# Kernel tuning notes

Measured on AMD Instinct MI355X. Metric: run time of the kernel, lower is better.

The kernel has to match this reference:

```python
import math
import jax, jax.numpy as jnp
import numpy as np

B = 2
N = 48           # max_atoms
A = 16           # num_atom_types
E = 5            # num_bond_types
HID = 384
NH = 8
HD = HID // NH   # 48
LYR = 4
MLP = 4 * HID
L = N + N * N    # 2352 sequence length (nodes + flattened edges)


def setup_inputs() -> dict:
    key = jax.random.key(0)
    ks = iter(jax.random.split(key, 48))
    r = lambda *s: jax.random.normal(next(ks), s, jnp.float32) * 0.02
    d = {
        "x": jax.random.normal(next(ks), (B, N, A), jnp.float32),
        "adj": jax.random.normal(next(ks), (B, N, N, E), jnp.float32),
        "t": jax.random.uniform(next(ks), (B,), jnp.float32),
        # embeddings
        "node_w": r(A, HID), "node_b": jnp.zeros((HID,), jnp.float32),
        "edge_w": r(E, HID), "edge_b": jnp.zeros((HID,), jnp.float32),
        "pos": r(L, HID),
        # timestep MLP (SinusoidalPositionalEmbedding(HID) -> Linear(HID,4H) -> SiLU -> Linear(4H,H))
        "t_w1": r(HID, 4 * HID), "t_b1": jnp.zeros((4 * HID,), jnp.float32),
        "t_w2": r(4 * HID, HID), "t_b2": jnp.zeros((HID,), jnp.float32),
        # stacked per-layer params
        "ada1_w": r(LYR, HID, 2 * HID), "ada1_b": jnp.zeros((LYR, 2 * HID), jnp.float32),
        "ada2_w": r(LYR, HID, 2 * HID), "ada2_b": jnp.zeros((LYR, 2 * HID), jnp.float32),
        "q_w": r(LYR, HID, HID), "q_b": jnp.zeros((LYR, HID), jnp.float32),
        "k_w": r(LYR, HID, HID), "k_b": jnp.zeros((LYR, HID), jnp.float32),
        "v_w": r(LYR, HID, HID), "v_b": jnp.zeros((LYR, HID), jnp.float32),
        "o_w": r(LYR, HID, HID), "o_b": jnp.zeros((LYR, HID), jnp.float32),
        "m1_w": r(LYR, HID, MLP), "m1_b": jnp.zeros((LYR, MLP), jnp.float32),
        "m2_w": r(LYR, MLP, HID), "m2_b": jnp.zeros((LYR, HID), jnp.float32),
        # final norm + heads (heads random instead of zero-init so output is informative)
        "fn_g": jnp.ones((HID,), jnp.float32), "fn_b": jnp.zeros((HID,), jnp.float32),
        "on_w": r(HID, A), "on_b": jnp.zeros((A,), jnp.float32),
        "oe_w": r(HID, E), "oe_b": jnp.zeros((E,), jnp.float32),
    }
    return d


def _ln(z):
    # LayerNorm(elementwise_affine=False), eps=1e-5
    mu = z.mean(-1, keepdims=True)
    var = z.var(-1, keepdims=True)
    return (z - mu) * jax.lax.rsqrt(var + 1e-5)


def _forward(x, adj, t, node_w, node_b, edge_w, edge_b, pos,
             t_w1, t_b1, t_w2, t_b2,
             ada1_w, ada1_b, ada2_w, ada2_b,
             q_w, q_b, k_w, k_b, v_w, v_b, o_w, o_b,
             m1_w, m1_b, m2_w, m2_b,
             fn_g, fn_b, on_w, on_b, oe_w, oe_b):
    b = x.shape[0]
    # embed nodes and edges, concat into sequence [b, L, HID]
    h_nodes = x @ node_w + node_b                       # [b, N, H]
    h_edges = adj.reshape(b, N * N, E) @ edge_w + edge_b  # [b, N*N, H]
    h = jnp.concatenate([h_nodes, h_edges], axis=1) + pos[None]
    # sinusoidal timestep embedding -> cond [b, HID]
    half = HID // 2
    freqs = jnp.exp(-math.log(10000.0) * jnp.arange(half, dtype=jnp.float32) / half)
    ang = t[:, None].astype(jnp.float32) * freqs[None, :]
    temb = jnp.concatenate([jnp.sin(ang), jnp.cos(ang)], axis=-1)
    cond = jax.nn.silu(temb @ t_w1 + t_b1) @ t_w2 + t_b2
    inv_scale = 1.0 / math.sqrt(HD)
    for i in range(LYR):
        # AdaLN 1 + attention
        sc, sh = jnp.split(cond @ ada1_w[i] + ada1_b[i], 2, axis=-1)
        n = _ln(h) * (1.0 + sc[:, None, :]) + sh[:, None, :]
        q = (n @ q_w[i] + q_b[i]).reshape(b, L, NH, HD)
        k = (n @ k_w[i] + k_b[i]).reshape(b, L, NH, HD)
        v = (n @ v_w[i] + v_b[i]).reshape(b, L, NH, HD)
        scores = jnp.einsum('bqhd,bkhd->bhqk', q, k) * inv_scale
        attn = jax.nn.softmax(scores, axis=-1)
        ao = jnp.einsum('bhqk,bkhd->bqhd', attn, v).reshape(b, L, HID)
        h = h + ao @ o_w[i] + o_b[i]
        # AdaLN 2 + MLP (exact GELU as in nn.GELU default)
        sc2, sh2 = jnp.split(cond @ ada2_w[i] + ada2_b[i], 2, axis=-1)
        n2 = _ln(h) * (1.0 + sc2[:, None, :]) + sh2[:, None, :]
        h = h + jax.nn.gelu(n2 @ m1_w[i] + m1_b[i], approximate=False) @ m2_w[i] + m2_b[i]
    h = _ln(h) * fn_g + fn_b
    node_out = h[:, :N] @ on_w + on_b                   # [b, N, A]
    edge_out = (h[:, N:] @ oe_w + oe_b).reshape(b, N, N, E)
    return node_out, edge_out


def reference(x, adj, t, node_w, node_b, edge_w, edge_b, pos,
              t_w1, t_b1, t_w2, t_b2,
              ada1_w, ada1_b, ada2_w, ada2_b,
              q_w, q_b, k_w, k_b, v_w, v_b, o_w, o_b,
              m1_w, m1_b, m2_w, m2_b,
              fn_g, fn_b, on_w, on_b, oe_w, oe_b):
    return _forward(x, adj, t, node_w, node_b, edge_w, edge_b, pos,
                    t_w1, t_b1, t_w2, t_b2,
                    ada1_w, ada1_b, ada2_w, ada2_b,
                    q_w, q_b, k_w, k_b, v_w, v_b, o_w, o_b,
                    m1_w, m1_b, m2_w, m2_b,
                    fn_g, fn_b, on_w, on_b, oe_w, oe_b)
```

## Files before the change

kernel.cpp:

```cpp
#include <hip/hip_runtime.h>
#include <hip/hip_bf16.h>
#include <math.h>

typedef __hip_bfloat16 bf16;
typedef __attribute__((ext_vector_type(8))) short short8;
typedef __attribute__((ext_vector_type(4))) float f32x4;

#define B_ 2
#define N_ 48
#define A_ 16
#define E_ 5
#define HID 384
#define NHD 8
#define HD 48
#define LYR 4
#define MLPD 1536
#define L_ 2352
#define M_ 4704
#define VLP 2432
#define QSCALE 0.20823513f

#define WQ_  0LL
#define WK_  589824LL
#define WV_  1179648LL
#define WO_  1769472LL
#define WM1_ 2359296LL
#define WM2_ 4718592LL
#define WTOT 7077888
#define BQ_  0
#define BK_  1536
#define BV_  3072
#define BO_  4608
#define BM1_ 6144
#define BM2_ 12288
#define BTOT 13824

static __device__ __forceinline__ float b2f(bf16 v) { return __bfloat162float(v); }
static __device__ __forceinline__ float us2f(unsigned short u) {
    return __uint_as_float(((unsigned)u) << 16);
}
static __device__ __forceinline__ unsigned short f2us(float f) {
    bf16 h = __float2bfloat16(f);
    return *reinterpret_cast<unsigned short*>(&h);
}
static __device__ __forceinline__ float ldv(const float* p, size_t i) { return p[i]; }
static __device__ __forceinline__ float ldv(const bf16*  p, size_t i) { return b2f(p[i]); }
static __device__ __forceinline__ void  stv(float* p, size_t i, float v) { p[i] = v; }
static __device__ __forceinline__ void  stv(bf16*  p, size_t i, float v) { p[i] = __float2bfloat16(v); }
static __device__ __forceinline__ float4 ld4(const float* p, size_t i) {
    return *reinterpret_cast<const float4*>(p + i);
}
static __device__ __forceinline__ float4 ld4(const bf16* p, size_t i) {
    ushort4 u = *reinterpret_cast<const ushort4*>(p + i);
    return make_float4(us2f(u.x), us2f(u.y), us2f(u.z), us2f(u.w));
}

__global__ void k_detect(const void* w, int* flag) {
    if (threadIdx.x == 0 && blockIdx.x == 0) {
        const bf16* p = (const bf16*)w;
        int isf = 0;
        for (int i = 0; i < 256; ++i) {
            float v = fabsf(b2f(p[i]));
            if (!(v <= 1000.0f)) { isf = 1; break; }
        }
        *flag = isf;
    }
}

template <typename T>
static __device__ void prepw_body(
    const T* q_w, const T* k_w, const T* v_w, const T* o_w,
    const T* m1_w, const T* m2_w, bf16* wbt)
{
    __shared__ unsigned short Ts[64][72];
    const int z = blockIdx.y;
    const int kind = z >> 2, l = z & 3;
    const T* src; int K, N; long long dbase;
    switch (kind) {
        case 0: src = q_w;  K = 384;  N = 384;  dbase = WQ_;  break;
        case 1: src = k_w;  K = 384;  N = 384;  dbase = WK_;  break;
        case 2: src = v_w;  K = 384;  N = 384;  dbase = WV_;  break;
        case 3: src = o_w;  K = 384;  N = 384;  dbase = WO_;  break;
        case 4: src = m1_w; K = 384;  N = 1536; dbase = WM1_; break;
        default: src = m2_w; K = 1536; N = 384; dbase = WM2_; break;
    }
    const int Nt = N >> 6;
    const int tiles = (K >> 6) * Nt;
    if (blockIdx.x >= tiles) return;
    const int tk = blockIdx.x / Nt, tn = blockIdx.x % Nt;
    const int k0 = tk*64, n0 = tn*64;
    const size_t soff = (size_t)l * K * N;
    const size_t doff = (size_t)dbase + (size_t)l * K * N;
    const int tid = threadIdx.x;
    {
        const int kk = tid >> 2, nc = (tid & 3) * 16;
        #pragma unroll
        for (int j = 0; j < 16; ++j)
            Ts[kk][nc + j] = f2us(ldv(src, soff + (size_t)(k0 + kk)*N + n0 + nc + j));
    }
    __syncthreads();
    {
        const int nn = tid >> 2, kc = (tid & 3) * 16;
        unsigned short tmp[16];
        #pragma unroll
        for (int j = 0; j < 16; ++j) tmp[j] = Ts[kc + j][nn];
        unsigned short* dst = (unsigned short*)wbt + doff + (size_t)(n0 + nn)*K + k0 + kc;
        *reinterpret_cast<short8*>(dst)     = *reinterpret_cast<short8*>(&tmp[0]);
        *reinterpret_cast<short8*>(dst + 8) = *reinterpret_cast<short8*>(&tmp[8]);
    }
}

__global__ __launch_bounds__(256) void k_prepw(
    const void* q_w, const void* k_w, const void* v_w, const void* o_w,
    const void* m1_w, const void* m2_w, const int* __restrict__ fl, bf16* __restrict__ wbt)
{
    if (*fl) prepw_body<float>((const float*)q_w, (const float*)k_w, (const float*)v_w,
                               (const float*)o_w, (const float*)m1_w, (const float*)m2_w, wbt);
    else     prepw_body<bf16>((const bf16*)q_w, (const bf16*)k_w, (const bf16*)v_w,
                              (const bf16*)o_w, (const bf16*)m1_w, (const bf16*)m2_w, wbt);
}

template <typename T>
static __device__ void prepb_body(
    const T* q_b, const T* k_b, const T* v_b, const T* o_b,
    const T* m1_b, const T* m2_b, bf16* bb)
{
    for (int i = threadIdx.x; i < BTOT; i += 256) {
        float v;
        if      (i < BK_)  v = ldv(q_b,  i);
        else if (i < BV_)  v = ldv(k_b,  i - BK_);
        else if (i < BO_)  v = ldv(v_b,  i - BV_);
        else if (i < BM1_) v = ldv(o_b,  i - BO_);
        else if (i < BM2_) v = ldv(m1_b, i - BM1_);
        else               v = ldv(m2_b, i - BM2_);
        bb[i] = __float2bfloat16(v);
    }
}

__global__ __launch_bounds__(256) void k_prepb(
    const void* q_b, const void* k_b, const void* v_b, const void* o_b,
    const void* m1_b, const void* m2_b, const int* __restrict__ fl, bf16* __restrict__ bb)
{
    if (*fl) prepb_body<float>((const float*)q_b, (const float*)k_b, (const float*)v_b,
                               (const float*)o_b, (const float*)m1_b, (const float*)m2_b, bb);
    else     prepb_body<bf16>((const bf16*)q_b, (const bf16*)k_b, (const bf16*)v_b,
                              (const bf16*)o_b, (const bf16*)m1_b, (const bf16*)m2_b, bb);
}

template <typename T>
static __device__ void embed_body(
    const T* x, const T* adj, const T* node_w, const T* node_b,
    const T* edge_w, const T* edge_b, const T* pos, float* h)
{
    const int bl = blockIdx.x;
    const int b = bl / L_, l = bl % L_;
    const int c = threadIdx.x;
    float acc;
    if (l < N_) {
        acc = ldv(node_b, c);
        const size_t xr = (size_t)(b*N_ + l)*A_;
        #pragma unroll
        for (int a = 0; a < A_; ++a) acc += ldv(x, xr + a) * ldv(node_w, (size_t)a*HID + c);
    } else {
        const int e = l - N_;
        acc = ldv(edge_b, c);
        const size_t ar = ((size_t)b*N_*N_ + e)*E_;
        #pragma unroll
        for (int j = 0; j < E_; ++j) acc += ldv(adj, ar + j) * ldv(edge_w, (size_t)j*HID + c);
    }
    h[(size_t)bl*HID + c] = acc + ldv(pos, (size_t)l*HID + c);
}

__global__ __launch_bounds__(384) void k_embed(
    const void* x, const void* adj, const void* node_w, const void* node_b,
    const void* edge_w, const void* edge_b, const void* pos,
    const int* __restrict__ fl, float* __restrict__ h)
{
    if (*fl) embed_body<float>((const float*)x, (const float*)adj, (const float*)node_w,
                               (const float*)node_b, (const float*)edge_w, (const float*)edge_b,
                               (const float*)pos, h);
    else     embed_body<bf16>((const bf16*)x, (const bf16*)adj, (const bf16*)node_w,
                              (const bf16*)node_b, (const bf16*)edge_w, (const bf16*)edge_b,
                              (const bf16*)pos, h);
}

template <typename T>
static __device__ void cond1_body(const T* t, const T* t_w1, const T* t_b1, float* hid)
{
    __shared__ float temb[HID];
    __shared__ float red[4][64];
    const int b = blockIdx.x, jb = blockIdx.y, tid = threadIdx.x;
    const float tv = ldv(t, b);
    for (int c = tid; c < HID; c += 256) {
        int i = (c < 192) ? c : c - 192;
        float f = expf(-9.2103403719761836f * (float)i / 192.0f);
        float ang = tv * f;
        temb[c] = (c < 192) ? sinf(ang) : cosf(ang);
    }
    __syncthreads();
    const int ko = tid >> 6, jo = tid & 63;
    const int j = jb*64 + jo;
    float acc = 0.f;
    for (int i = ko*96; i < (ko + 1)*96; ++i)
        acc += temb[i] * ldv(t_w1, (size_t)i*4*HID + j);
    red[ko][jo] = acc;
    __syncthreads();
    if (ko == 0) {
        float a = red[0][jo] + red[1][jo] + red[2][jo] + red[3][jo] + ldv(t_b1, j);
        hid[(size_t)b*4*HID + j] = a / (1.0f + expf(-a));
    }
}

__global__ __launch_bounds__(256) void k_cond1(
    const void* t, const void* t_w1, const void* t_b1,
    const int* __restrict__ fl, float* __restrict__ hid)
{
    if (*fl) cond1_body<float>((const float*)t, (const float*)t_w1, (const float*)t_b1, hid);
    else     cond1_body<bf16>((const bf16*)t, (const bf16*)t_w1, (const bf16*)t_b1, hid);
}

template <typename T>
static __device__ void cond2_body(const T* t_w2, const T* t_b2, const float* hid, float* part)
{
    __shared__ float hs[128];
    const int b = blockIdx.x, ch = blockIdx.y, c = threadIdx.x;
    const int j0 = ch*128;
    if (c < 128) hs[c] = hid[(size_t)b*4*HID + j0 + c];
    __syncthreads();
    float acc = (ch == 0) ? ldv(t_b2, c) : 0.f;
    for (int jj = 0; jj < 128; ++jj)
        acc += hs[jj] * ldv(t_w2, (size_t)(j0 + jj)*HID + c);
    part[((size_t)b*12 + ch)*HID + c] = acc;
}

__global__ __launch_bounds__(384) void k_cond2(
    const void* t_w2, const void* t_b2, const int* __restrict__ fl,
    const float* __restrict__ hid, float* __restrict__ part)
{
    if (*fl) cond2_body<float>((const float*)t_w2, (const float*)t_b2, hid, part);
    else     cond2_body<bf16>((const bf16*)t_w2, (const bf16*)t_b2, hid, part);
}

template <typename T>
static __device__ void cond3_body(
    const T* ada1_w, const T* ada1_b, const T* ada2_w, const T* ada2_b,
    const float* part, float* ada_out)
{
    __shared__ float cs[HID];
    const int slot = blockIdx.x / 3, ob = blockIdx.x % 3, b = blockIdx.y;
    const int tid = threadIdx.x;
    for (int c = tid; c < HID; c += 256) {
        float s = 0.f;
        #pragma unroll
        for (int ch = 0; ch < 12; ++ch) s += part[((size_t)b*12 + ch)*HID + c];
        cs[c] = s;
    }
    __syncthreads();
    const int layer = slot >> 1, which = slot & 1;
    const int o = ob*256 + tid;
    const T* W  = which ? ada2_w : ada1_w;
    const T* Bi = which ? ada2_b : ada1_b;
    float acc = ldv(Bi, (size_t)layer*768 + o);
    const size_t wb = (size_t)layer*HID*768 + o;
    for (int c = 0; c < HID; ++c) acc += cs[c] * ldv(W, wb + (size_t)c*768);
    ada_out[((size_t)slot*B_ + b)*768 + o] = acc;
}

__global__ __launch_bounds__(256) void k_cond3(
    const void* ada1_w, const void* ada1_b, const void* ada2_w, const void* ada2_b,
    const int* __restrict__ fl, const float* __restrict__ part, float* __restrict__ ada_out)
{
    if (*fl) cond3_body<float>((const float*)ada1_w, (const float*)ada1_b,
                               (const float*)ada2_w, (const float*)ada2_b, part, ada_out);
    else     cond3_body<bf16>((const bf16*)ada1_w, (const bf16*)ada1_b,
                              (const bf16*)ada2_w, (const bf16*)ada2_b, part, ada_out);
}

__global__ __launch_bounds__(256) void k_adaln(
    const float* __restrict__ h, const float* __restrict__ ada,
    bf16* __restrict__ n, int slot)
{
    const int row  = blockIdx.x * 4 + (threadIdx.x >> 6);
    const int lane = threadIdx.x & 63;
    const int b = row / L_;
    const float* hr = h + (size_t)row*HID;
    float v[6]; float s = 0.f, ss = 0.f;
    #pragma unroll
    for (int j = 0; j < 6; ++j) { float t = hr[lane + j*64]; v[j] = t; s += t; ss += t*t; }
    #pragma unroll
    for (int off = 32; off; off >>= 1) { s += __shfl_xor(s, off); ss += __shfl_xor(ss, off); }
    const float mu = s * (1.0f/HID);
    const float rs = rsqrtf(fmaxf(ss * (1.0f/HID) - mu*mu, 0.0f) + 1e-5f);
    const float* ap = ada + ((size_t)slot*B_ + b)*768;
    bf16* nr = n + (size_t)row*HID;
    #pragma unroll
    for (int j = 0; j < 6; ++j) {
        int c = lane + j*64;
        nr[c] = __float2bfloat16((v[j] - mu)*rs*(1.0f + ap[c]) + ap[384 + c]);
    }
}

static __device__ __forceinline__ void gemm_epilogue(
    f32x4 (&acc)[2][2], float bcol0, float bcol1,
    bf16* Cb, float* Cf, int M, int N, int act, int mode,
    int bm, int bn, int wm, int wn, int quad, int c)
{
    const float bcol[2] = {bcol0, bcol1};
    #pragma unroll
    for (int mi = 0; mi < 2; ++mi)
        #pragma unroll
        for (int ni = 0; ni < 2; ++ni) {
            const int col = bn + wn*32 + ni*16 + c;
            #pragma unroll
            for (int r = 0; r < 4; ++r) {
                const int row = bm + wm*32 + mi*16 + quad*4 + r;
                if (row < M) {
                    float v = acc[mi][ni][r] + bcol[ni];
                    if (act) v = 0.5f * v * (1.0f + erff(v * 0.70710678118654752f));
                    if (mode == 1) Cf[(size_t)row*N + col] += v;
                    else if (mode == 0) Cb[(size_t)row*N + col] = __float2bfloat16(v);
                    else if (mode == 3) Cb[(size_t)row*N + col] = __float2bfloat16(v * QSCALE);
                    else {
                        const int b   = row >= L_ ? 1 : 0;
                        const int key = row - b*L_;
                        const int hh  = col / 48, d = col - hh*48;
                        Cb[((size_t)(b*8 + hh)*48 + d)*VLP + key] = __float2bfloat16(v);
                    }
                }
            }
        }
}

template <typename T>
static __device__ void gemm_body(
    const bf16* A, const T* W, long long woff, const T* bias, long long boff,
    bf16* Cb, float* Cf, int M, int N, int K, int act, int mode)
{
    __shared__ __align__(16) unsigned short As[64][72];
    __shared__ __align__(16) unsigned short Bt[64][72];
    const int tid  = threadIdx.x;
    const int wv   = tid >> 6, lane = tid & 63;
    const int quad = lane >> 4, c = lane & 15;
    const int wm = wv & 1, wn = wv >> 1;
    const int bm = blockIdx.x * 64, bn = blockIdx.y * 64;
    const int arow = tid >> 3, ach = tid & 7;
    f32x4 acc[2][2] = {{{0.f,0.f,0.f,0.f},{0.f,0.f,0.f,0.f}},
                       {{0.f,0.f,0.f,0.f},{0.f,0.f,0.f,0.f}}};
    for (int k0 = 0; k0 < K; k0 += 64) {
        short8 av[2]; float4 w0[2], w1[2];
        #pragma unroll
        for (int i = 0; i < 2; ++i) {
            const int row = i*32 + arow;
            av[i] = short8{0,0,0,0,0,0,0,0};
            if (bm + row < M)
                av[i] = *reinterpret_cast<const short8*>(
                            A + (size_t)(bm + row)*K + k0 + ach*8);
            const size_t wrow = (size_t)woff + (size_t)(k0 + i*32 + arow)*N + bn + ach*8;
            w0[i] = ld4(W, wrow);
            w1[i] = ld4(W, wrow + 4);
        }
        __syncthreads();
        #pragma unroll
        for (int i = 0; i < 2; ++i) {
            *reinterpret_cast<short8*>(&As[i*32 + arow][ach*8]) = av[i];
            const int kk = i*32 + arow, nb0 = ach*8;
            Bt[nb0+0][kk] = f2us(w0[i].x); Bt[nb0+1][kk] = f2us(w0[i].y);
            Bt[nb0+2][kk] = f2us(w0[i].z); Bt[nb0+3][kk] = f2us(w0[i].w);
            Bt[nb0+4][kk] = f2us(w1[i].x); Bt[nb0+5][kk] = f2us(w1[i].y);
            Bt[nb0+6][kk] = f2us(w1[i].z); Bt[nb0+7][kk] = f2us(w1[i].w);
        }
        __syncthreads();
        #pragma unroll
        for (int ks = 0; ks < 2; ++ks) {
            short8 af[2], bfr[2];
            #pragma unroll
            for (int mi = 0; mi < 2; ++mi)
                af[mi] = *reinterpret_cast<const short8*>(
                             &As[wm*32 + mi*16 + c][ks*32 + quad*8]);
            #pragma unroll
            for (int ni = 0; ni < 2; ++ni)
                bfr[ni] = *reinterpret_cast<const short8*>(
                              &Bt[wn*32 + ni*16 + c][ks*32 + quad*8]);
            #pragma unroll
            for (int mi = 0; mi < 2; ++mi)
                #pragma unroll
                for (int ni = 0; ni < 2; ++ni)
                    acc[mi][ni] = __builtin_amdgcn_mfma_f32_16x16x32_bf16(
                                      af[mi], bfr[ni], acc[mi][ni], 0, 0, 0);
        }
    }
    gemm_epilogue(acc, ldv(bias, (size_t)boff + bn + wn*32 + c),
                  ldv(bias, (size_t)boff + bn + wn*32 + 16 + c),
                  Cb, Cf, M, N, act, mode, bm, bn, wm, wn, quad, c);
}

__global__ __launch_bounds__(256) void k_gemm(
    const bf16* __restrict__ A, const void* W, long long woff, const void* bias, long long boff,
    bf16* Cb, float* Cf, int M, int N, int K, int act, int mode,
    const int* __restrict__ fl)
{
    if (*fl) gemm_body<float>(A, (const float*)W, woff, (const float*)bias, boff,
                              Cb, Cf, M, N, K, act, mode);
    else     gemm_body<bf16>(A, (const bf16*)W, woff, (const bf16*)bias, boff,
                             Cb, Cf, M, N, K, act, mode);
}

__global__ __launch_bounds__(256) void k_gemm_qkv(
    const bf16* __restrict__ A,
    const void* qw, const void* kw, const void* vw,
    const void* qb, const void* kb, const void* vb,
    long long woff, long long boff,
    bf16* Cq, bf16* Ck, bf16* Cv, const int* __restrict__ fl)
{
    const int z = blockIdx.z;
    const void* W  = (z == 0) ? qw : (z == 1) ? kw : vw;
    const void* Bi = (z == 0) ? qb : (z == 1) ? kb : vb;
    bf16* C        = (z == 0) ? Cq : (z == 1) ? Ck : Cv;
    const int mode = (z == 0) ? 3 : (z == 2) ? 2 : 0;
    if (*fl) gemm_body<float>(A, (const float*)W, woff, (const float*)Bi, boff,
                              C, nullptr, M_, HID, HID, 0, mode);
    else     gemm_body<bf16>(A, (const bf16*)W, woff, (const bf16*)Bi, boff,
                             C, nullptr, M_, HID, HID, 0, mode);
}

static __device__ void gemm_t_body(
    const bf16* A, const bf16* Wt, long long woff, const bf16* bias, long long boff,
    bf16* Cb, float* Cf, int M, int N, int K, int act, int mode)
{
    __shared__ __align__(16) unsigned short As[64][72];
    __shared__ __align__(16) unsigned short Bt[64][72];
    const int tid  = threadIdx.x;
    const int wv   = tid >> 6, lane = tid & 63;
    const int quad = lane >> 4, c = lane & 15;
    const int wm = wv & 1, wn = wv >> 1;
    const int bm = blockIdx.x * 64, bn = blockIdx.y * 64;
    const int arow = tid >> 3, ach = tid & 7;
    f32x4 acc[2][2] = {{{0.f,0.f,0.f,0.f},{0.f,0.f,0.f,0.f}},
                       {{0.f,0.f,0.f,0.f},{0.f,0.f,0.f,0.f}}};
    for (int k0 = 0; k0 < K; k0 += 64) {
        short8 av[2], wv8[2];
        #pragma unroll
        for (int i = 0; i < 2; ++i) {
            const int row = i*32 + arow;
            av[i] = short8{0,0,0,0,0,0,0,0};
            if (bm + row < M)
                av[i] = *reinterpret_cast<const short8*>(
                            A + (size_t)(bm + row)*K + k0 + ach*8);
            wv8[i] = *reinterpret_cast<const short8*>(
                         Wt + (size_t)woff + (size_t)(bn + row)*K + k0 + ach*8);
        }
        __syncthreads();
        #pragma unroll
        for (int i = 0; i < 2; ++i) {
            *reinterpret_cast<short8*>(&As[i*32 + arow][ach*8]) = av[i];
            *reinterpret_cast<short8*>(&Bt[i*32 + arow][ach*8]) = wv8[i];
        }
        __syncthreads();
        #pragma unroll
        for (int ks = 0; ks < 2; ++ks) {
            short8 af[2], bfr[2];
            #pragma unroll
            for (int mi = 0; mi < 2; ++mi)
                af[mi] = *reinterpret_cast<const short8*>(
                             &As[wm*32 + mi*16 + c][ks*32 + quad*8]);
            #pragma unroll
            for (int ni = 0; ni < 2; ++ni)
                bfr[ni] = *reinterpret_cast<const short8*>(
                              &Bt[wn*32 + ni*16 + c][ks*32 + quad*8]);
            #pragma unroll
            for (int mi = 0; mi < 2; ++mi)
                #pragma unroll
                for (int ni = 0; ni < 2; ++ni)
                    acc[mi][ni] = __builtin_amdgcn_mfma_f32_16x16x32_bf16(
                                      af[mi], bfr[ni], acc[mi][ni], 0, 0, 0);
        }
    }
    gemm_epilogue(acc, b2f(bias[boff + bn + wn*32 + c]),
                  b2f(bias[boff + bn + wn*32 + 16 + c]),
                  Cb, Cf, M, N, act, mode, bm, bn, wm, wn, quad, c);
}

__global__ __launch_bounds__(256) void k_gemm_t(
    const bf16* __restrict__ A, const bf16* __restrict__ Wt, long long woff,
    const bf16* __restrict__ bias, long long boff,
    bf16* Cb, float* Cf, int M, int N, int K, int act, int mode)
{
    gemm_t_body(A, Wt, woff, bias, boff, Cb, Cf, M, N, K, act, mode);
}

__global__ __launch_bounds__(256) void k_gemm_qkv_t(
    const bf16* __restrict__ A, const bf16* __restrict__ wbt, const bf16* __restrict__ bb,
    int lyr, bf16* Cq, bf16* Ck, bf16* Cv)
{
    const int z = blockIdx.z;
    long long woff; long long boff; bf16* C; int mode;
    if (z == 0)      { woff = WQ_ + (long long)lyr*147456; boff = BQ_ + lyr*384; C = Cq; mode = 3; }
    else if (z == 1) { woff = WK_ + (long long)lyr*147456; boff = BK_ + lyr*384; C = Ck; mode = 0; }
    else             { woff = WV_ + (long long)lyr*147456; boff = BV_ + lyr*384; C = Cv; mode = 2; }
    gemm_t_body(A, wbt, woff, bb, boff, C, nullptr, M_, HID, HID, 0, mode);
}

__global__ __launch_bounds__(512) void k_attn(
    const bf16* __restrict__ q, const bf16* __restrict__ k,
    const bf16* __restrict__ vt, bf16* __restrict__ ao)
{
    __shared__ __align__(16) unsigned short Ks[2][64][80];
    __shared__ __align__(16) unsigned short Vt[2][48][72];
    __shared__ __align__(16) unsigned short Pq[8][16][72];
    const int tid  = threadIdx.x;
    const int w    = tid >> 6, lane = tid & 63;
    const int quad = lane >> 4, c = lane & 15;
    const int qt = w & 3, sp = w >> 2;
    const int bh = blockIdx.y;
    const size_t base  = (size_t)(bh >> 3)*L_*HID + (size_t)(bh & 7)*HD;
    const size_t vbase = (size_t)bh*48*VLP;
    const int q0 = blockIdx.x*64 + qt*16;
    const bool qvalid = q0 < L_;
    const int qrow = qvalid ? (q0 + c) : c;

    short8 qf0, qf1;
    {
        const unsigned short* qp = (const unsigned short*)(q + base + (size_t)qrow*HID);
        qf0 = *reinterpret_cast<const short8*>(qp + quad*8);
        if (quad < 2) qf1 = *reinterpret_cast<const short8*>(qp + 32 + quad*8);
        else          qf1 = short8{0,0,0,0,0,0,0,0};
    }
    f32x4 o0 = {0.f,0.f,0.f,0.f}, o1 = {0.f,0.f,0.f,0.f}, o2 = {0.f,0.f,0.f,0.f};
    float m = -3.0e38f, lsum = 0.f;

    const int t256 = tid & 255, grp = tid >> 8;
    const int krow0 = t256 >> 3, kch = t256 & 7;
    const int krow1 = 32 + krow0;
    const int vd0 = krow0;
    const int vd1 = 32 + (krow0 & 15);
    const bool vl1 = (t256 < 128);
    const unsigned short* kq = (const unsigned short*)(k + base);
    const unsigned short* vq = (const unsigned short*)(vt + vbase);
    const short8 Z8 = short8{0,0,0,0,0,0,0,0};
    short8 kr0 = Z8, kr1 = Z8, vr0, vr1 = Z8;
    {
        const int kb0 = grp*1216;
        if (kch < 6) {
            kr0 = *reinterpret_cast<const short8*>(kq + (size_t)(kb0 + krow0)*HID + kch*8);
            kr1 = *reinterpret_cast<const short8*>(kq + (size_t)(kb0 + krow1)*HID + kch*8);
        }
        vr0 = *reinterpret_cast<const short8*>(vq + (size_t)vd0*VLP + kb0 + kch*8);
        if (vl1) vr1 = *reinterpret_cast<const short8*>(vq + (size_t)vd1*VLP + kb0 + kch*8);
    }

    for (int tt = 0; tt < 19; ++tt) {
        __syncthreads();
        *reinterpret_cast<short8*>(&Ks[grp][krow0][kch*8]) = kr0;
        *reinterpret_cast<short8*>(&Ks[grp][krow1][kch*8]) = kr1;
        *reinterpret_cast<short8*>(&Vt[grp][vd0][kch*8])   = vr0;
        if (vl1) *reinterpret_cast<short8*>(&Vt[grp][vd1][kch*8]) = vr1;
        __syncthreads();
        if (tt < 18) {
            const int nb0 = grp*1216 + (tt + 1)*64;
            if (kch < 6) {
                kr0 = *reinterpret_cast<const short8*>(kq + (size_t)(nb0 + krow0)*HID + kch*8);
                kr1 = *reinterpret_cast<const short8*>(kq + (size_t)(nb0 + krow1)*HID + kch*8);
            }
            vr0 = *reinterpret_cast<const short8*>(vq + (size_t)vd0*VLP + nb0 + kch*8);
            if (vl1) vr1 = *reinterpret_cast<const short8*>(vq + (size_t)vd1*VLP + nb0 + kch*8);
        }

        const int kt = sp*1216 + tt*64;
        float sv[16];
        #pragma unroll
        for (int t = 0; t < 4; ++t) {
            f32x4 acc = {0.f,0.f,0.f,0.f};
            short8 a0 = *reinterpret_cast<const short8*>(&Ks[sp][t*16 + c][quad*8]);
            short8 a1 = *reinterpret_cast<const short8*>(&Ks[sp][t*16 + c][32 + quad*8]);
            acc = __builtin_amdgcn_mfma_f32_16x16x32_bf16(a0, qf0, acc, 0, 0, 0);
            acc = __builtin_amdgcn_mfma_f32_16x16x32_bf16(a1, qf1, acc, 0, 0, 0);
            #pragma unroll
            for (int r = 0; r < 4; ++r) sv[t*4 + r] = acc[r];
        }
        if (sp == 1 && tt >= 17) {
            #pragma unroll
            for (int t = 0; t < 4; ++t)
                #pragma unroll
                for (int r = 0; r < 4; ++r)
                    if (kt + t*16 + quad*4 + r >= L_) sv[t*4 + r] = -3.0e38f;
        }
        float tmax = sv[0];
        #pragma unroll
        for (int i = 1; i < 16; ++i) tmax = fmaxf(tmax, sv[i]);
        tmax = fmaxf(tmax, __shfl_xor(tmax, 16));
        tmax = fmaxf(tmax, __shfl_xor(tmax, 32));
        const float mn = fmaxf(m, tmax);
        const float alpha = exp2f(m - mn);
        m = mn;
        float psum = 0.f;
        unsigned short pv[16];
        #pragma unroll
        for (int i = 0; i < 16; ++i) {
            const float p = exp2f(sv[i] - m);
            psum += p;
            pv[i] = f2us(p);
        }
        lsum = lsum * alpha + psum;
        o0 *= alpha; o1 *= alpha; o2 *= alpha;
        #pragma unroll
        for (int t = 0; t < 4; ++t)
            *reinterpret_cast<ushort4*>(&Pq[w][c][t*16 + quad*4]) =
                make_ushort4(pv[t*4+0], pv[t*4+1], pv[t*4+2], pv[t*4+3]);
        #pragma unroll
        for (int s = 0; s < 2; ++s) {
            short8 pf  = *reinterpret_cast<const short8*>(&Pq[w][c][s*32 + quad*8]);
            short8 vf0 = *reinterpret_cast<const short8*>(&Vt[sp][c][s*32 + quad*8]);
            short8 vf1 = *reinterpret_cast<const short8*>(&Vt[sp][16 + c][s*32 + quad*8]);
            short8 vf2 = *reinterpret_cast<const short8*>(&Vt[sp][32 + c][s*32 + quad*8]);
            o0 = __builtin_amdgcn_mfma_f32_16x16x32_bf16(vf0, pf, o0, 0, 0, 0);
            o1 = __builtin_amdgcn_mfma_f32_16x16x32_bf16(vf1, pf, o1, 0, 0, 0);
            o2 = __builtin_amdgcn_mfma_f32_16x16x32_bf16(vf2, pf, o2, 0, 0, 0);
        }
    }
    float lw = lsum;
    lw += __shfl_xor(lw, 16);
    lw += __shfl_xor(lw, 32);
    float* Mg = (float*)&Ks[0][0][0];
    __syncthreads();
    if (sp == 1) {
        float* dst = Mg + (size_t)(qt*64 + lane)*14;
        dst[0] = o0[0]; dst[1] = o0[1]; dst[2]  = o0[2]; dst[3]  = o0[3];
        dst[4] = o1[0]; dst[5] = o1[1]; dst[6]  = o1[2]; dst[7]  = o1[3];
        dst[8] = o2[0]; dst[9] = o2[1]; dst[10] = o2[2]; dst[11] = o2[3];
        dst[12] = m; dst[13] = lw;
    }
    __syncthreads();
    if (sp == 0 && qvalid) {
        const float* src = Mg + (size_t)(qt*64 + lane)*14;
        const float m2 = src[12], l2 = src[13];
        const float mm = fmaxf(m, m2);
        const float a1 = exp2f(m - mm), a2 = exp2f(m2 - mm);
        const float inv = 1.0f / (lw*a1 + l2*a2);
        unsigned short* orow = (unsigned short*)(ao + base + (size_t)(q0 + c)*HID);
        const f32x4 ot[3] = {o0, o1, o2};
        #pragma unroll
        for (int dt = 0; dt < 3; ++dt) {
            ushort4 w4;
            w4.x = f2us((ot[dt][0]*a1 + src[dt*4+0]*a2) * inv);
            w4.y = f2us((ot[dt][1]*a1 + src[dt*4+1]*a2) * inv);
            w4.z = f2us((ot[dt][2]*a1 + src[dt*4+2]*a2) * inv);
            w4.w = f2us((ot[dt][3]*a1 + src[dt*4+3]*a2) * inv);
            *reinterpret_cast<ushort4*>(orow + dt*16 + quad*4) = w4;
        }
    }
}

template <typename T, typename TO>
static __device__ void final_body(
    const float* h, const T* fn_g, const T* fn_b,
    const T* on_w, const T* on_b, const T* oe_w, const T* oe_b, TO* out)
{
    __shared__ float hf[HID];
    const int row = blockIdx.x;
    const int b = row / L_, l = row % L_;
    const int lane = threadIdx.x;
    const float* hr = h + (size_t)row*HID;
    float v[6]; float s = 0.f, ss = 0.f;
    #pragma unroll
    for (int j = 0; j < 6; ++j) { float t = hr[lane + j*64]; v[j] = t; s += t; ss += t*t; }
    #pragma unroll
    for (int off = 32; off; off >>= 1) { s += __shfl_xor(s, off); ss += __shfl_xor(ss, off); }
    const float mu = s * (1.0f/HID);
    const float rs = rsqrtf(fmaxf(ss * (1.0f/HID) - mu*mu, 0.0f) + 1e-5f);
    #pragma unroll
    for (int j = 0; j < 6; ++j) {
        int c = lane + j*64;
        hf[c] = (v[j] - mu) * rs * ldv(fn_g, c) + ldv(fn_b, c);
    }
    __syncthreads();
    if (l < N_) {
        if (lane < A_) {
            float acc = ldv(on_b, lane);
            for (int c = 0; c < HID; ++c) acc += hf[c] * ldv(on_w, (size_t)c*A_ + lane);
            stv(out, (size_t)(b*N_ + l)*A_ + lane, acc);
        }
    } else {
        const int e = l - N_;
        if (lane < E_) {
            float acc = ldv(oe_b, lane);
            for (int c = 0; c < HID; ++c) acc += hf[c] * ldv(oe_w, (size_t)c*E_ + lane);
            stv(out, (size_t)B_*N_*A_ + ((size_t)b*N_*N_ + e)*E_ + lane, acc);
        }
    }
}

__global__ __launch_bounds__(64) void k_final(
    const float* __restrict__ h, const void* fn_g, const void* fn_b,
    const void* on_w, const void* on_b, const void* oe_w, const void* oe_b,
    const int* __restrict__ fl, void* out)
{
    if (*fl) final_body<float, float>(h, (const float*)fn_g, (const float*)fn_b,
                                      (const float*)on_w, (const float*)on_b,
                                      (const float*)oe_w, (const float*)oe_b, (float*)out);
    else     final_body<bf16, bf16>(h, (const bf16*)fn_g, (const bf16*)fn_b,
                                    (const bf16*)on_w, (const bf16*)on_b,
                                    (const bf16*)oe_w, (const bf16*)oe_b, (bf16*)out);
}

extern "C" void kernel_launch(void* const* d_in, const int* in_sizes, int n_in,
                              void* d_out, int out_size, void* d_ws, size_t ws_size,
                              hipStream_t stream) {
    const void* x      = d_in[0];
    const void* adj    = d_in[1];
    const void* t      = d_in[2];
    const void* node_w = d_in[3];
    const void* node_b = d_in[4];
    const void* edge_w = d_in[5];
    const void* edge_b = d_in[6];
    const void* pos    = d_in[7];
    const void* t_w1   = d_in[8];
    const void* t_b1   = d_in[9];
    const void* t_w2   = d_in[10];
    const void* t_b2   = d_in[11];
    const void* ada1_w = d_in[12];
    const void* ada1_b = d_in[13];
    const void* ada2_w = d_in[14];
    const void* ada2_b = d_in[15];
    const void* q_w    = d_in[16];
    const void* q_b    = d_in[17];
    const void* k_w    = d_in[18];
    const void* k_b    = d_in[19];
    const void* v_w    = d_in[20];
    const void* v_b    = d_in[21];
    const void* o_w    = d_in[22];
    const void* o_b    = d_in[23];
    const void* m1_w   = d_in[24];
    const void* m1_b   = d_in[25];
    const void* m2_w   = d_in[26];
    const void* m2_b   = d_in[27];
    const void* fn_g   = d_in[28];
    const void* fn_b   = d_in[29];
    const void* on_w   = d_in[30];
    const void* on_b   = d_in[31];
    const void* oe_w   = d_in[32];
    const void* oe_b   = d_in[33];

    const size_t SZ  = (size_t)M_ * HID;
    const size_t VTZ = (size_t)B_*NHD*HD*VLP;
    const size_t FLT = SZ + 12288 + (size_t)B_*4*HID + (size_t)B_*12*HID;
    const size_t M1FULL = (size_t)M_ * MLPD;
    const size_t BF_BASE = 3*SZ + VTZ;
    const size_t BF_BIG  = SZ + M1FULL;
    const size_t NEED      = 256 + sizeof(float)*FLT + sizeof(bf16)*BF_BASE;
    const size_t NEED_BIG  = 256 + sizeof(float)*FLT + sizeof(bf16)*BF_BIG;
    const size_t NEED_PREP = 256 + sizeof(float)*FLT
                           + sizeof(bf16)*(BF_BIG + WTOT + BTOT);
    if (ws_size < NEED) {
        hipMemsetAsync(d_out, 0, (size_t)out_size*sizeof(bf16), stream);
        return;
    }
    const bool big  = (ws_size >= NEED_BIG);
    const bool prep = (ws_size >= NEED_PREP);
    int*   fl   = (int*)d_ws;
    float* h    = (float*)((char*)d_ws + 256);
    float* ada  = h + SZ;
    float* hid  = ada + 12288;
    float* part = hid + (size_t)B_*4*HID;
    bf16* nb  = (bf16*)(part + (size_t)B_*12*HID);
    bf16* qb  = nb + SZ;
    bf16* kb  = qb + SZ;
    bf16* vtb = kb + SZ;
    bf16* m1c = kb;
    bf16* m1f = qb;
    bf16* wbt = nb + BF_BIG;
    bf16* bb  = wbt + WTOT;

    k_detect<<<1, 64, 0, stream>>>(node_w, fl);
    if (prep) {
        k_prepw<<<dim3(144, 24), 256, 0, stream>>>(q_w, k_w, v_w, o_w, m1_w, m2_w, fl, wbt);
        k_prepb<<<1, 256, 0, stream>>>(q_b, k_b, v_b, o_b, m1_b, m2_b, fl, bb);
    }
    k_embed<<<M_, HID, 0, stream>>>(x, adj, node_w, node_b, edge_w, edge_b, pos, fl, h);
    k_cond1<<<dim3(B_, 24), 256, 0, stream>>>(t, t_w1, t_b1, fl, hid);
    k_cond2<<<dim3(B_, 12), 384, 0, stream>>>(t_w2, t_b2, fl, hid, part);
    k_cond3<<<dim3(24, B_), 256, 0, stream>>>(ada1_w, ada1_b, ada2_w, ada2_b, fl, part, ada);
    for (int i = 0; i < LYR; ++i) {
        const long long woff   = (long long)i * HID * HID;
        const long long boff   = (long long)i * HID;
        const long long m1woff = (long long)i * HID * MLPD;
        const long long m1boff = (long long)i * MLPD;
        const long long m2woff = (long long)i * MLPD * HID;

        k_adaln<<<M_/4, 256, 0, stream>>>(h, ada, nb, 2*i);
        if (prep) {
            k_gemm_qkv_t<<<dim3(74, 6, 3), 256, 0, stream>>>(nb, wbt, bb, i, qb, kb, vtb);
            k_attn<<<dim3(37, B_*NHD), 512, 0, stream>>>(qb, kb, vtb, nb);
            k_gemm_t<<<dim3(74, 6), 256, 0, stream>>>(nb, wbt, WO_ + (long long)i*147456,
                                                      bb, BO_ + i*384,
                                                      nullptr, h, M_, HID, HID, 0, 1);
            k_adaln<<<M_/4, 256, 0, stream>>>(h, ada, nb, 2*i + 1);
            k_gemm_t<<<dim3(74, 24), 256, 0, stream>>>(nb, wbt, WM1_ + (long long)i*589824,
                                                       bb, BM1_ + i*MLPD,
                                                       m1f, nullptr, M_, MLPD, HID, 1, 0);
            k_gemm_t<<<dim3(74, 6), 256, 0, stream>>>(m1f, wbt, WM2_ + (long long)i*589824,
                                                      bb, BM2_ + i*384,
                                                      nullptr, h, M_, HID, MLPD, 0, 1);
        } else {
            k_gemm_qkv<<<dim3(74, 6, 3), 256, 0, stream>>>(nb, q_w, k_w, v_w, q_b, k_b, v_b,
                                                           woff, boff, qb, kb, vtb, fl);
            k_attn<<<dim3(37, B_*NHD), 512, 0, stream>>>(qb, kb, vtb, nb);
            k_gemm<<<dim3(74, 6), 256, 0, stream>>>(nb, o_w, woff, o_b, boff,
                                                    nullptr, h, M_, HID, HID, 0, 1, fl);
            k_adaln<<<M_/4, 256, 0, stream>>>(h, ada, nb, 2*i + 1);
            if (big) {
                k_gemm<<<dim3(74, 24), 256, 0, stream>>>(nb, m1_w, m1woff, m1_b, m1boff,
                                                         m1f, nullptr, M_, MLPD, HID, 1, 0, fl);
                k_gemm<<<dim3(74, 6), 256, 0, stream>>>(m1f, m2_w, m2woff, m2_b, boff,
                                                        nullptr, h, M_, HID, MLPD, 0, 1, fl);
            } else {
                for (int c = 0; c < 2; ++c) {
                    k_gemm<<<dim3(37, 24), 256, 0, stream>>>(nb + (size_t)c*2352*HID,
                                                             m1_w, m1woff, m1_b, m1boff,
                                                             m1c, nullptr, 2352, MLPD, HID, 1, 0, fl);
                    k_gemm<<<dim3(37, 6), 256, 0, stream>>>(m1c, m2_w, m2woff, m2_b, boff,
                                                            nullptr, h + (size_t)c*2352*HID,
                                                            2352, HID, MLPD, 0, 1, fl);
                }
            }
        }
    }
    k_final<<<M_, 64, 0, stream>>>(h, fn_g, fn_b, on_w, on_b, oe_w, oe_b, fl, (void*)d_out);
}
```

Baseline: 854.2 us.

## Split-K O-proj and MLP2 GEMMs with atomics, prefetch tiles, lazy softmax rescale

Adds a split-K GEMM variant that accumulates partial products into the fp32 residual with atomicAdd, and uses it for the output projection (2-way) and the second MLP GEMM (3-way) so those narrow-N launches fill more compute units. The transposed-weight GEMM body now register-prefetches the next K tile while computing the current one. The attention kernel uses a tree max reduction and skips the online-softmax rescale unless the running max grows by more than a threshold. The costs are atomic traffic and order-dependent fp32 accumulation, plus possible loss of precision from the lazy rescale.

After: 872.3 us. +2.1%, slower.

```diff
diff --git a/kernel.cpp b/kernel.cpp
--- a/kernel.cpp
+++ b/kernel.cpp
@@ -318,6 +318,7 @@
                     float v = acc[mi][ni][r] + bcol[ni];
                     if (act) v = 0.5f * v * (1.0f + erff(v * 0.70710678118654752f));
                     if (mode == 1) Cf[(size_t)row*N + col] += v;
+                    else if (mode == 4) atomicAdd(&Cf[(size_t)row*N + col], v);
                     else if (mode == 0) Cb[(size_t)row*N + col] = __float2bfloat16(v);
                     else if (mode == 3) Cb[(size_t)row*N + col] = __float2bfloat16(v * QSCALE);
                     else {
@@ -425,7 +426,8 @@
 
 static __device__ void gemm_t_body(
     const bf16* A, const bf16* Wt, long long woff, const bf16* bias, long long boff,
-    bf16* Cb, float* Cf, int M, int N, int K, int act, int mode)
+    bf16* Cb, float* Cf, int M, int N, int K, int act, int mode,
+    int bn, int kb, int ke, int bias_en)
 {
     __shared__ __align__(16) unsigned short As[64][72];
     __shared__ __align__(16) unsigned short Bt[64][72];
@@ -433,22 +435,24 @@
     const int wv   = tid >> 6, lane = tid & 63;
     const int quad = lane >> 4, c = lane & 15;
     const int wm = wv & 1, wn = wv >> 1;
-    const int bm = blockIdx.x * 64, bn = blockIdx.y * 64;
+    const int bm = blockIdx.x * 64;
     const int arow = tid >> 3, ach = tid & 7;
     f32x4 acc[2][2] = {{{0.f,0.f,0.f,0.f},{0.f,0.f,0.f,0.f}},
                        {{0.f,0.f,0.f,0.f},{0.f,0.f,0.f,0.f}}};
-    for (int k0 = 0; k0 < K; k0 += 64) {
-        short8 av[2], wv8[2];
+    short8 av[2], wv8[2];
+    {
         #pragma unroll
         for (int i = 0; i < 2; ++i) {
             const int row = i*32 + arow;
             av[i] = short8{0,0,0,0,0,0,0,0};
             if (bm + row < M)
                 av[i] = *reinterpret_cast<const short8*>(
-                            A + (size_t)(bm + row)*K + k0 + ach*8);
+                            A + (size_t)(bm + row)*K + kb + ach*8);
             wv8[i] = *reinterpret_cast<const short8*>(
-                         Wt + (size_t)woff + (size_t)(bn + row)*K + k0 + ach*8);
-        }
+                         Wt + (size_t)woff + (size_t)(bn + row)*K + kb + ach*8);
+        }
+    }
+    for (int k0 = kb; k0 < ke; k0 += 64) {
         __syncthreads();
         #pragma unroll
         for (int i = 0; i < 2; ++i) {
@@ -456,6 +460,19 @@
             *reinterpret_cast<short8*>(&Bt[i*32 + arow][ach*8]) = wv8[i];
         }
         __syncthreads();
+        if (k0 + 64 < ke) {
+            const int kn = k0 + 64;
+            #pragma unroll
+            for (int i = 0; i < 2; ++i) {
+                const int row = i*32 + arow;
+                av[i] = short8{0,0,0,0,0,0,0,0};
+                if (bm + row < M)
+                    av[i] = *reinterpret_cast<const short8*>(
+                                A + (size_t)(bm + row)*K + kn + ach*8);
+                wv8[i] = *reinterpret_cast<const short8*>(
+                             Wt + (size_t)woff + (size_t)(bn + row)*K + kn + ach*8);
+            }
+        }
         #pragma unroll
         for (int ks = 0; ks < 2; ++ks) {
             short8 af[2], bfr[2];
@@ -475,8 +492,9 @@
                                       af[mi], bfr[ni], acc[mi][ni], 0, 0, 0);
         }
     }
-    gemm_epilogue(acc, b2f(bias[boff + bn + wn*32 + c]),
-                  b2f(bias[boff + bn + wn*32 + 16 + c]),
+    const float bs = bias_en ? 1.0f : 0.0f;
+    gemm_epilogue(acc, bs * b2f(bias[boff + bn + wn*32 + c]),
+                  bs * b2f(bias[boff + bn + wn*32 + 16 + c]),
                   Cb, Cf, M, N, act, mode, bm, bn, wm, wn, quad, c);
 }
 
@@ -485,7 +503,21 @@
     const bf16* __restrict__ bias, long long boff,
     bf16* Cb, float* Cf, int M, int N, int K, int act, int mode)
 {
-    gemm_t_body(A, Wt, woff, bias, boff, Cb, Cf, M, N, K, act, mode);
+    gemm_t_body(A, Wt, woff, bias, boff, Cb, Cf, M, N, K, act, mode,
+                blockIdx.y*64, 0, K, 1);
+}
+
+__global__ __launch_bounds__(256) void k_gemm_t_sk(
+    const bf16* __restrict__ A, const bf16* __restrict__ Wt, long long woff,
+    const bf16* __restrict__ bias, long long boff,
+    float* __restrict__ Cf, int M, int N, int K, int nsplit)
+{
+    const int ntiles = N >> 6;
+    const int nt = (int)blockIdx.y % ntiles;
+    const int sp = (int)blockIdx.y / ntiles;
+    const int kc = K / nsplit;
+    gemm_t_body(A, Wt, woff, bias, boff, nullptr, Cf, M, N, K, 0, 4,
+                nt*64, sp*kc, (sp + 1)*kc, sp == 0);
 }
 
 __global__ __launch_bounds__(256) void k_gemm_qkv_t(
@@ -497,7 +529,8 @@
     if (z == 0)      { woff = WQ_ + (long long)lyr*147456; boff = BQ_ + lyr*384; C = Cq; mode = 3; }
     else if (z == 1) { woff = WK_ + (long long)lyr*147456; boff = BK_ + lyr*384; C = Ck; mode = 0; }
     else             { woff = WV_ + (long long)lyr*147456; boff = BV_ + lyr*384; C = Cv; mode = 2; }
-    gemm_t_body(A, wbt, woff, bb, boff, C, nullptr, M_, HID, HID, 0, mode);
+    gemm_t_body(A, wbt, woff, bb, boff, C, nullptr, M_, HID, HID, 0, mode,
+                blockIdx.y*64, 0, HID, 1);
 }
 
 __global__ __launch_bounds__(512) void k_attn(
@@ -584,14 +617,20 @@
                 for (int r = 0; r < 4; ++r)
                     if (kt + t*16 + quad*4 + r >= L_) sv[t*4 + r] = -3.0e38f;
         }
-        float tmax = sv[0];
-        #pragma unroll
-        for (int i = 1; i < 16; ++i) tmax = fmaxf(tmax, sv[i]);
+        float tmax = fmaxf(fmaxf(fmaxf(sv[0], sv[1]),  fmaxf(sv[2],  sv[3])),
+                           fmaxf(fmaxf(sv[4], sv[5]),  fmaxf(sv[6],  sv[7])));
+        float tmx2 = fmaxf(fmaxf(fmaxf(sv[8], sv[9]),  fmaxf(sv[10], sv[11])),
+                           fmaxf(fmaxf(sv[12], sv[13]), fmaxf(sv[14], sv[15])));
+        tmax = fmaxf(tmax, tmx2);
         tmax = fmaxf(tmax, __shfl_xor(tmax, 16));
         tmax = fmaxf(tmax, __shfl_xor(tmax, 32));
-        const float mn = fmaxf(m, tmax);
-        const float alpha = exp2f(m - mn);
-        m = mn;
+        if (!__all(tmax <= m + 8.0f)) {
+            const float mn = fmaxf(m, tmax);
+            const float alpha = exp2f(m - mn);
+            m = mn;
+            lsum *= alpha;
+            o0 *= alpha; o1 *= alpha; o2 *= alpha;
+        }
         float psum = 0.f;
         unsigned short pv[16];
         #pragma unroll
@@ -600,8 +639,7 @@
             psum += p;
             pv[i] = f2us(p);
         }
-        lsum = lsum * alpha + psum;
-        o0 *= alpha; o1 *= alpha; o2 *= alpha;
+        lsum += psum;
         #pragma unroll
         for (int t = 0; t < 4; ++t)
             *reinterpret_cast<ushort4*>(&Pq[w][c][t*16 + quad*4]) =
@@ -790,16 +828,16 @@
         if (prep) {
             k_gemm_qkv_t<<<dim3(74, 6, 3), 256, 0, stream>>>(nb, wbt, bb, i, qb, kb, vtb);
             k_attn<<<dim3(37, B_*NHD), 512, 0, stream>>>(qb, kb, vtb, nb);
-            k_gemm_t<<<dim3(74, 6), 256, 0, stream>>>(nb, wbt, WO_ + (long long)i*147456,
-                                                      bb, BO_ + i*384,
-                                                      nullptr, h, M_, HID, HID, 0, 1);
+            k_gemm_t_sk<<<dim3(74, 12), 256, 0, stream>>>(nb, wbt, WO_ + (long long)i*147456,
+                                                          bb, BO_ + i*384,
+                                                          h, M_, HID, HID, 2);
             k_adaln<<<M_/4, 256, 0, stream>>>(h, ada, nb, 2*i + 1);
             k_gemm_t<<<dim3(74, 24), 256, 0, stream>>>(nb, wbt, WM1_ + (long long)i*589824,
                                                        bb, BM1_ + i*MLPD,
                                                        m1f, nullptr, M_, MLPD, HID, 1, 0);
-            k_gemm_t<<<dim3(74, 6), 256, 0, stream>>>(m1f, wbt, WM2_ + (long long)i*589824,
-                                                      bb, BM2_ + i*384,
-                                                      nullptr, h, M_, HID, MLPD, 0, 1);
+            k_gemm_t_sk<<<dim3(74, 18), 256, 0, stream>>>(m1f, wbt, WM2_ + (long long)i*589824,
+                                                          bb, BM2_ + i*384,
+                                                          h, M_, HID, MLPD, 3);
         } else {
             k_gemm_qkv<<<dim3(74, 6, 3), 256, 0, stream>>>(nb, q_w, k_w, v_w, q_b, k_b, v_b,
                                                            woff, boff, qb, kb, vtb, fl);
```
